# Optimization experiments

Hardware: AMD Instinct MI355X
Metric: run time of the kernel (lower is better)

The kernel has to match this reference:

```python
import jax, jax.numpy as jnp
import numpy as np

M, K, N, GROUP = 64, 4096, 14336, 128
G = K // GROUP  # 32 groups along the input dim


def setup_inputs() -> dict:
    key = jax.random.key(0)
    ks = jax.random.split(key, 8)
    # int8 activations (stored as int32 for jax convenience, values in [-128,127])
    x = jax.random.randint(ks[0], (M, K), -128, 128, dtype=jnp.int32)
    # unpacked uint4 weights: values in [0,15], logical layout [N, K]
    qweight = jax.random.randint(ks[1], (N, K), 0, 16, dtype=jnp.int32)
    # per-group int8 second-level scales (positive) and pre-multiplied zeros = -zero*scale
    s2_scales = jax.random.randint(ks[2], (G, N), 1, 8, dtype=jnp.int32)
    zeros = jax.random.randint(ks[3], (G, N), 0, 16, dtype=jnp.int32)
    s2_zeros = (-zeros * s2_scales).astype(jnp.int32)
    # per-output-channel fp scales and per-token dynamic activation scales
    s1_scales = jax.random.uniform(ks[4], (N,), jnp.float32, 1e-3, 1e-2)
    input_scales = jax.random.uniform(ks[5], (M,), jnp.float32, 1e-3, 2e-2)
    # input_sum is an arg of forward_per_group but unused by the per-group kernel
    input_sum = jnp.sum(x, axis=1).astype(jnp.float32)
    bias = jax.random.normal(ks[6], (N,), jnp.float32) * 0.01
    return {"x": x, "input_scales": input_scales, "input_sum": input_sum,
            "qweight": qweight, "s2_scales": s2_scales, "s2_zeros": s2_zeros,
            "s1_scales": s1_scales, "bias": bias}


def reference(x, input_scales, input_sum, qweight, s2_scales, s2_zeros, s1_scales, bias):
    # W4A8 per-group GEMM: dequant int4 weight per group of GROUP input channels:
    #   w_int8[o,k] = q4[o,k] * s2_scales[g,o] + s2_zeros[g,o]   (g = k // GROUP)
    # acc[m,o] = sum_k x_int8[m,k] * w_int8[o,k]
    # out[m,o] = acc * input_scales[m] * s1_scales[o] + bias[o]
    m, k = x.shape
    n = qweight.shape[0]
    g = s2_scales.shape[0]
    gs = k // g
    xg = x.reshape(m, g, gs).astype(jnp.float32)          # [M,G,gs]
    qg = qweight.reshape(n, g, gs).astype(jnp.float32)    # [N,G,gs]
    partial = jnp.einsum('mgk,ogk->mgo', xg, qg)          # per-group int partial sums
    xsum = xg.sum(axis=-1)                                # [M,G]
    acc = (jnp.einsum('mgo,go->mo', partial, s2_scales.astype(jnp.float32))
           + jnp.einsum('mg,go->mo', xsum, s2_zeros.astype(jnp.float32)))
    out = acc * input_scales[:, None] * s1_scales[None, :] + bias[None, :]
    return out
```

## Files before the change

### kernel.cpp

```cpp
#include <hip/hip_runtime.h>


typedef int v4i __attribute__((ext_vector_type(4)));

#define MM 64
#define KK 4096
#define NN 14336
#define GG 32
#define BN 64
#define BK 64
#define NT (KK / BK)

__global__ __launch_bounds__(256) void w4a8_gemm_kernel(
    const int* __restrict__ x,
    const float* __restrict__ input_scales,
    const int* __restrict__ qweight,
    const int* __restrict__ s2_scales,
    const int* __restrict__ s2_zeros,
    const float* __restrict__ s1_scales,
    const float* __restrict__ bias,
    float* __restrict__ out)
{
    __shared__ int x_lds[64 * 17];
    __shared__ int w_lds[64 * 17];
    __shared__ int s2_lds[GG * BN];
    __shared__ int z_lds[GG * BN];

    const int t  = threadIdx.x;
    const int n0 = blockIdx.x * BN;

    for (int i = t; i < GG * BN; i += 256) {
        int g = i >> 6;
        int n = i & 63;
        s2_lds[i] = s2_scales[g * NN + n0 + n];
        z_lds[i]  = s2_zeros [g * NN + n0 + n];
    }
    __syncthreads();

    const int rbase = t >> 4;
    const int c4    = t & 15;

    v4i qv[4], xv[4];
    #pragma unroll
    for (int j = 0; j < 4; ++j) {
        int r = rbase + 16 * j;
        qv[j] = *(const v4i*)(qweight + (size_t)(n0 + r) * KK + c4 * 4);
        xv[j] = *(const v4i*)(x       + (size_t)r        * KK + c4 * 4);
    }

    const int lane = t & 63;
    const int wv   = t >> 6;
    const int arow = lane & 15;
    const int kq   = lane >> 4;

    v4i acc[4];
    #pragma unroll
    for (int q = 0; q < 4; ++q) acc[q] = (v4i){0, 0, 0, 0};

    for (int it = 0; it < NT; ++it) {
        const int g = it >> 1;

        #pragma unroll
        for (int j = 0; j < 4; ++j) {
            int r = rbase + 16 * j;
            int s2v = s2_lds[g * 64 + r];
            int zv  = z_lds [g * 64 + r];
            v4i q4 = qv[j];
            int w0 = q4.x * s2v + zv;
            int w1 = q4.y * s2v + zv;
            int w2 = q4.z * s2v + zv;
            int w3 = q4.w * s2v + zv;
            unsigned pw = (unsigned)(w0 & 255)
                        | ((unsigned)(w1 & 255) << 8)
                        | ((unsigned)(w2 & 255) << 16)
                        | ((unsigned)w3 << 24);
            w_lds[r * 17 + c4] = (int)pw;

            v4i x4 = xv[j];
            unsigned px = (unsigned)(x4.x & 255)
                        | ((unsigned)(x4.y & 255) << 8)
                        | ((unsigned)(x4.z & 255) << 16)
                        | ((unsigned)x4.w << 24);
            x_lds[r * 17 + c4] = (int)px;
        }

        if (it + 1 < NT) {
            #pragma unroll
            for (int j = 0; j < 4; ++j) {
                int r = rbase + 16 * j;
                qv[j] = *(const v4i*)(qweight + (size_t)(n0 + r) * KK + (it + 1) * BK + c4 * 4);
                xv[j] = *(const v4i*)(x       + (size_t)r        * KK + (it + 1) * BK + c4 * 4);
            }
        }

        __syncthreads();

        v4i bv;
        {
            int base = (wv * 16 + arow) * 17 + kq * 4;
            bv.x = w_lds[base + 0];
            bv.y = w_lds[base + 1];
            bv.z = w_lds[base + 2];
            bv.w = w_lds[base + 3];
        }
        #pragma unroll
        for (int q = 0; q < 4; ++q) {
            int base = (q * 16 + arow) * 17 + kq * 4;
            v4i av;
            av.x = x_lds[base + 0];
            av.y = x_lds[base + 1];
            av.z = x_lds[base + 2];
            av.w = x_lds[base + 3];
            acc[q] = __builtin_amdgcn_mfma_i32_16x16x64_i8(av, bv, acc[q], 0, 0, 0);
        }

        __syncthreads();
    }

    const int n = n0 + wv * 16 + arow;
    const float s1b = s1_scales[n];
    const float bb  = bias[n];
    #pragma unroll
    for (int q = 0; q < 4; ++q) {
        #pragma unroll
        for (int r = 0; r < 4; ++r) {
            int m = q * 16 + kq * 4 + r;
            float v = (float)acc[q][r] * input_scales[m] * s1b + bb;
            out[(size_t)m * NN + n] = v;
        }
    }
}

extern "C" void kernel_launch(void* const* d_in, const int* in_sizes, int n_in,
                              void* d_out, int out_size, void* d_ws, size_t ws_size,
                              hipStream_t stream) {
    const int*   xx    = (const int*)d_in[0];
    const float* iscal = (const float*)d_in[1];
    const int*   qw    = (const int*)d_in[3];
    const int*   s2s   = (const int*)d_in[4];
    const int*   s2z   = (const int*)d_in[5];
    const float* s1    = (const float*)d_in[6];
    const float* bb    = (const float*)d_in[7];
    float* outp = (float*)d_out;

    hipLaunchKernelGGL(w4a8_gemm_kernel, dim3(NN / BN), dim3(256), 0, stream,
                       xx, iscal, qw, s2s, s2z, s1, bb, outp);
}
```

Before: 346.7 us.

## Split-K the W4A8 GEMM into 4 slices with separate epilogue reduction kernel

Splits the K dimension into four chunks across a second grid dimension, so there are 4x as many blocks (224 to 896) to fill the GPU's compute units. Each block writes int32 partial sums to workspace, and a new epilogue kernel sums the four partials and applies the scales and bias. Weight loads use nontemporal hints and launch bounds request 4 blocks per CU. The trade-off is extra workspace traffic (four 64x14336 int planes) and a second kernel launch.

```diff
diff --git a/kernel.cpp b/kernel.cpp
--- a/kernel.cpp
+++ b/kernel.cpp
@@ -6,36 +6,36 @@
 #define MM 64
 #define KK 4096
 #define NN 14336
-#define GG 32
 #define BN 64
 #define BK 64
-#define NT (KK / BK)
+#define KS 4
+#define KCH (KK / KS)
+#define NT (KCH / BK)
+#define GPB (KCH / 128)
 
-__global__ __launch_bounds__(256) void w4a8_gemm_kernel(
+__global__ __launch_bounds__(256, 4) void w4a8_gemm_kernel(
     const int* __restrict__ x,
-    const float* __restrict__ input_scales,
     const int* __restrict__ qweight,
     const int* __restrict__ s2_scales,
     const int* __restrict__ s2_zeros,
-    const float* __restrict__ s1_scales,
-    const float* __restrict__ bias,
-    float* __restrict__ out)
+    int* __restrict__ partial)
 {
     __shared__ int x_lds[64 * 17];
     __shared__ int w_lds[64 * 17];
-    __shared__ int s2_lds[GG * BN];
-    __shared__ int z_lds[GG * BN];
+    __shared__ int s2_lds[GPB * BN];
+    __shared__ int z_lds[GPB * BN];
 
     const int t  = threadIdx.x;
     const int n0 = blockIdx.x * BN;
+    const int ks = blockIdx.y;
+    const int k0 = ks * KCH;
 
-    for (int i = t; i < GG * BN; i += 256) {
+    for (int i = t; i < GPB * BN; i += 256) {
         int g = i >> 6;
         int n = i & 63;
-        s2_lds[i] = s2_scales[g * NN + n0 + n];
-        z_lds[i]  = s2_zeros [g * NN + n0 + n];
+        s2_lds[i] = s2_scales[(size_t)(ks * GPB + g) * NN + n0 + n];
+        z_lds[i]  = s2_zeros [(size_t)(ks * GPB + g) * NN + n0 + n];
     }
-    __syncthreads();
 
     const int rbase = t >> 4;
     const int c4    = t & 15;
@@ -44,9 +44,12 @@
     #pragma unroll
     for (int j = 0; j < 4; ++j) {
         int r = rbase + 16 * j;
-        qv[j] = *(const v4i*)(qweight + (size_t)(n0 + r) * KK + c4 * 4);
-        xv[j] = *(const v4i*)(x       + (size_t)r        * KK + c4 * 4);
+        qv[j] = __builtin_nontemporal_load(
+                    (const v4i*)(qweight + (size_t)(n0 + r) * KK + k0 + c4 * 4));
+        xv[j] = *(const v4i*)(x + (size_t)r * KK + k0 + c4 * 4);
     }
+
+    __syncthreads();
 
     const int lane = t & 63;
     const int wv   = t >> 6;
@@ -88,8 +91,9 @@
             #pragma unroll
             for (int j = 0; j < 4; ++j) {
                 int r = rbase + 16 * j;
-                qv[j] = *(const v4i*)(qweight + (size_t)(n0 + r) * KK + (it + 1) * BK + c4 * 4);
-                xv[j] = *(const v4i*)(x       + (size_t)r        * KK + (it + 1) * BK + c4 * 4);
+                qv[j] = __builtin_nontemporal_load(
+                            (const v4i*)(qweight + (size_t)(n0 + r) * KK + k0 + (it + 1) * BK + c4 * 4));
+                xv[j] = *(const v4i*)(x + (size_t)r * KK + k0 + (it + 1) * BK + c4 * 4);
             }
         }
 
@@ -118,17 +122,46 @@
     }
 
     const int n = n0 + wv * 16 + arow;
-    const float s1b = s1_scales[n];
-    const float bb  = bias[n];
+    int* pbase = partial + (size_t)ks * MM * NN;
     #pragma unroll
     for (int q = 0; q < 4; ++q) {
         #pragma unroll
         for (int r = 0; r < 4; ++r) {
             int m = q * 16 + kq * 4 + r;
-            float v = (float)acc[q][r] * input_scales[m] * s1b + bb;
-            out[(size_t)m * NN + n] = v;
+            pbase[(size_t)m * NN + n] = acc[q][r];
         }
     }
+}
+
+__global__ __launch_bounds__(256) void w4a8_epilogue_kernel(
+    const int* __restrict__ partial,
+    const float* __restrict__ input_scales,
+    const float* __restrict__ s1_scales,
+    const float* __restrict__ bias,
+    float* __restrict__ out)
+{
+    const int idx = blockIdx.x * 256 + threadIdx.x;
+    const int npv = NN / 4;
+    const int m  = idx / npv;
+    const int n  = (idx - m * npv) * 4;
+    const size_t base  = (size_t)m * NN + n;
+    const size_t plane = (size_t)MM * NN;
+
+    v4i a0 = __builtin_nontemporal_load((const v4i*)(partial + 0 * plane + base));
+    v4i a1 = __builtin_nontemporal_load((const v4i*)(partial + 1 * plane + base));
+    v4i a2 = __builtin_nontemporal_load((const v4i*)(partial + 2 * plane + base));
+    v4i a3 = __builtin_nontemporal_load((const v4i*)(partial + 3 * plane + base));
+
+    const float is = input_scales[m];
+    const float4 s1 = *(const float4*)(s1_scales + n);
+    const float4 bb = *(const float4*)(bias + n);
+
+    float4 o;
+    o.x = (float)(a0.x + a1.x + a2.x + a3.x) * is * s1.x + bb.x;
+    o.y = (float)(a0.y + a1.y + a2.y + a3.y) * is * s1.y + bb.y;
+    o.z = (float)(a0.z + a1.z + a2.z + a3.z) * is * s1.z + bb.z;
+    o.w = (float)(a0.w + a1.w + a2.w + a3.w) * is * s1.w + bb.w;
+    *(float4*)(out + base) = o;
 }
 
 extern "C" void kernel_launch(void* const* d_in, const int* in_sizes, int n_in,
@@ -142,7 +175,10 @@
     const float* s1    = (const float*)d_in[6];
     const float* bb    = (const float*)d_in[7];
     float* outp = (float*)d_out;
+    int*   part = (int*)d_ws;
 
-    hipLaunchKernelGGL(w4a8_gemm_kernel, dim3(NN / BN), dim3(256), 0, stream,
-                       xx, iscal, qw, s2s, s2z, s1, bb, outp);
+    hipLaunchKernelGGL(w4a8_gemm_kernel, dim3(NN / BN, KS), dim3(256), 0, stream,
+                       xx, qw, s2s, s2z, part);
+    hipLaunchKernelGGL(w4a8_epilogue_kernel, dim3((MM * NN / 4) / 256), dim3(256), 0, stream,
+                       part, iscal, s1, bb, outp);
 }
```

Measured after the change: 329.3 us. 5.0% less time.
